# Performance work log

Measured on AMD Instinct MI355X. Metric: run time of the kernel, lower is better.

## Reference

```python
import jax, jax.numpy as jnp
import numpy as np

B, NV, HID, TDIM = 1024, 256, 256, 128
NODE_IN = 2 + 4 + TDIM  # coords + pos_enc(4) + time_emb


def _sinusoidal_pos_emb(t, dim):
    # standard SinusoidalPosEmb: cat(sin, cos) of t * exp(-i*log(1e4)/(half-1))
    half = dim // 2
    freqs = jnp.exp(-np.log(10000.0) * jnp.arange(half, dtype=t.dtype) / (half - 1))
    ang = t[:, None] * freqs[None, :]
    return jnp.concatenate([jnp.sin(ang), jnp.cos(ang)], axis=-1)  # [B, dim]


def setup_inputs() -> dict:
    key = jax.random.key(0)
    ks = jax.random.split(key, 10)
    s = lambda fan_in: 1.0 / np.sqrt(fan_in)
    return {
        "x": jax.random.normal(ks[0], (B, NV * 2), dtype=jnp.float32),
        "t": jax.random.uniform(ks[1], (B,), dtype=jnp.float32) * 1000.0,
        "time_w": jax.random.normal(ks[2], (TDIM, TDIM), dtype=jnp.float32) * s(TDIM),
        "time_b": jnp.zeros((TDIM,), dtype=jnp.float32),
        "W0": jax.random.normal(ks[3], (NODE_IN, HID), dtype=jnp.float32) * s(NODE_IN),
        "b0": jnp.zeros((HID,), dtype=jnp.float32),
        "W1": jax.random.normal(ks[4], (HID, HID), dtype=jnp.float32) * s(HID),
        "b1": jnp.zeros((HID,), dtype=jnp.float32),
        "W2": jax.random.normal(ks[5], (HID, HID), dtype=jnp.float32) * s(HID),
        "b2": jnp.zeros((HID,), dtype=jnp.float32),
    }


def reference(x, t, time_w, time_b, W0, b0, W1, b1, W2, b2):
    Bsz, D = x.shape
    n = D // 2
    coords = x.reshape(Bsz, n, 2)  # [B, n, 2]

    # cycle positional features (pos_enc_dim=4): sin/cos of vertex angle + 2nd harmonic
    pos = jnp.arange(n, dtype=x.dtype)
    theta = (2.0 * jnp.pi) * pos / n
    pe = jnp.stack([jnp.sin(theta), jnp.cos(theta), jnp.sin(2.0 * theta), jnp.cos(2.0 * theta)], axis=-1)
    pe = jnp.broadcast_to(pe[None], (Bsz, n, 4))

    # time MLP: SinusoidalPosEmb -> Linear -> SiLU, broadcast to every node of the graph
    temb = jax.nn.silu(_sinusoidal_pos_emb(t, time_w.shape[0]) @ time_w + time_b)  # [B, TDIM]
    temb = jnp.broadcast_to(temb[:, None, :], (Bsz, n, temb.shape[-1]))

    h = jnp.concatenate([coords, pe, temb], axis=-1)  # [B, n, NODE_IN]

    # GCN layers over cycle adjacency with self-loops, symmetric-normalized (deg=3 -> 1/3).
    # Cycle structure: neighbors are prev/next vertex within each polygon -> jnp.roll on axis 1.
    for W, b in ((W0, b0), (W1, b1), (W2, b2)):
        s = h @ W + b  # support = x W + b
        agg = (s + jnp.roll(s, 1, axis=1) + jnp.roll(s, -1, axis=1)) / 3.0
        h = jax.nn.silu(agg)

    # mean pooling per graph (scatter_mean over graph_index == mean over vertex axis here)
    return h.mean(axis=1)  # [B, HID]
```

## Files before the change

### kernel.cpp

```cpp
#include <hip/hip_runtime.h>
#include <cstdint>

typedef __attribute__((ext_vector_type(8)))  short bf16x8;
typedef __attribute__((ext_vector_type(16))) float f32x16;
typedef __attribute__((ext_vector_type(4)))  int   i32x4;

__device__ __forceinline__ unsigned short f2bf(float x) {
  unsigned u = __float_as_uint(x);
  u += 0x7fffu + ((u >> 16) & 1u);
  return (unsigned short)(u >> 16);
}
__device__ __forceinline__ unsigned pk2bf(float lo, float hi) {
#if defined(__has_builtin)
#if __has_builtin(__builtin_amdgcn_cvt_pk_bf16_f32)
  auto v = __builtin_amdgcn_cvt_pk_bf16_f32(lo, hi);
  unsigned u; __builtin_memcpy(&u, &v, 4); return u;
#else
  return ((unsigned)f2bf(hi) << 16) | (unsigned)f2bf(lo);
#endif
#else
  return ((unsigned)f2bf(hi) << 16) | (unsigned)f2bf(lo);
#endif
}
__device__ __forceinline__ float silu_f(float v) {
  return v * __builtin_amdgcn_rcpf(1.0f + __expf(-v));
}

__device__ __forceinline__ float xchg32(float A, float B, int q) {
#if defined(__has_builtin)
#if __has_builtin(__builtin_amdgcn_permlane32_swap)
  auto r = __builtin_amdgcn_permlane32_swap(__float_as_uint(A), __float_as_uint(B),
                                            false, false);
  return __uint_as_float(q ? r[0] : r[1]);
#else
  return __shfl_xor(q ? A : B, 32);
#endif
#else
  return __shfl_xor(q ? A : B, 32);
#endif
}

__global__ void pack_kernel(const float* __restrict__ W0, const float* __restrict__ W1,
                            const float* __restrict__ W2,
                            unsigned short* __restrict__ packW) {
  __shared__ float ldsF[16][257];
  const int s = blockIdx.x, tid = threadIdx.x;
  const float* W; int KT, kmax, base, kt;
  if (s < 9)       { W = W0; KT = 9;  kmax = 134; base = 0;      kt = s; }
  else if (s < 25) { W = W1; KT = 16; kmax = 256; base = 36864;  kt = s - 9; }
  else             { W = W2; KT = 16; kmax = 256; base = 102400; kt = s - 25; }
  const int k0 = kt * 16;
#pragma unroll
  for (int i = 0; i < 8; ++i) {
    const int idx = i * 512 + tid;
    const int kl = idx >> 8, col = idx & 255;
    const int kg = k0 + kl;
    ldsF[kl][col] = (kg < kmax) ? W[kg * 256 + col] * 0.33333334f : 0.0f;
  }
  __syncthreads();
  const int g = tid >> 7, t = (tid >> 6) & 1, lane = tid & 63;
  const int col = g * 64 + t * 32 + (lane & 31);
  const int kb = 8 * (lane >> 5);
  unsigned u0 = pk2bf(ldsF[kb + 0][col], ldsF[kb + 1][col]);
  unsigned u1 = pk2bf(ldsF[kb + 2][col], ldsF[kb + 3][col]);
  unsigned u2 = pk2bf(ldsF[kb + 4][col], ldsF[kb + 5][col]);
  unsigned u3 = pk2bf(ldsF[kb + 6][col], ldsF[kb + 7][col]);
  unsigned short* dst = packW + base + g * (KT * 1024) + t * (KT * 512) + kt * 512 + lane * 8;
  i32x4 v = { (int)u0, (int)u1, (int)u2, (int)u3 };
  *(i32x4*)dst = v;
}


template <int ELAYER, bool DF, bool DL>
__device__ __forceinline__ void epi_pair(
    const int p, const f32x16* accEpi, const int q,
    const float recvI0, const float recvI1, const float recvX,
    const float extP, const float extN,
    const int epiSub, unsigned short* __restrict__ hbuf,
    const int* rowAddr, float& psum) {
  const int t = p >> 3, rp = (p & 7) * 2;
  float y0, y1;
  {
    const int r = rp;
    float prev;
    if (r > 0) prev = accEpi[t][r - 1];
    else       prev = q ? (t ? recvI1 : recvI0) : (t ? recvX : extP);
    y0 = silu_f(prev + accEpi[t][r] + accEpi[t][r + 1]);
  }
  {
    const int r = rp + 1;
    float next;
    if (r < 15) next = accEpi[t][r + 1];
    else        next = q ? (t ? extN : recvX) : (t ? recvI1 : recvI0);
    y1 = silu_f(accEpi[t][r - 1] + accEpi[t][r] + next);
  }
  const bool c0 = !(DF && t == 0 && rp == 0 && q == 0);
  const bool c1 = !(DL && t == 1 && rp == 14 && q == 1);
  if constexpr (ELAYER == 2) {
    if (c0) psum += y0;
    if (c1) psum += y1;
  } else {
    const unsigned u = pk2bf(y0, y1);
    char* bp = (char*)hbuf + (2 * epiSub + t) * 16384;
    if (c0) *(unsigned short*)(bp + rowAddr[rp])     = (unsigned short)u;
    if (c1) *(unsigned short*)(bp + rowAddr[rp + 1]) = (unsigned short)(u >> 16);
  }
}

template <int KT, int ELAYER, bool DOEPI, bool DF, bool DL>
__device__ __forceinline__ void fblock(
    unsigned short* __restrict__ hbuf, const int readSub, const int epiSub,
    const bf16x8* Bf, const int q, const int c, const float bias3,
    f32x16* accOut, const f32x16* accEpi,
    const float extP, const float extN,
    const int* rowAddr, float& psum) {
  float recvI0 = 0.f, recvI1 = 0.f, recvX = 0.f;
  if constexpr (DOEPI) {
    recvI0 = xchg32(accEpi[0][0],  accEpi[0][15], q);
    recvI1 = xchg32(accEpi[1][0],  accEpi[1][15], q);
    recvX  = xchg32(accEpi[0][15], accEpi[1][0],  q);
  }
#pragma unroll
  for (int t2 = 0; t2 < 2; ++t2)
#pragma unroll
    for (int j = 0; j < 16; ++j) accOut[t2][j] = bias3;
  const unsigned short* rb = hbuf + readSub * 16384 + c * 256;
#pragma unroll
  for (int kt = 0; kt < KT; ++kt) {
    const unsigned short* base = rb + (((2 * kt + q) ^ c) * 8);
    const bf16x8 a0 = *(const bf16x8*)(base);
    const bf16x8 a1 = *(const bf16x8*)(base + 8192);
    accOut[0] = __builtin_amdgcn_mfma_f32_32x32x16_bf16(a0, Bf[kt], accOut[0], 0, 0, 0);
    accOut[1] = __builtin_amdgcn_mfma_f32_32x32x16_bf16(a1, Bf[kt], accOut[1], 0, 0, 0);
    if constexpr (DOEPI) {
#pragma unroll
      for (int p = (kt * 16) / KT; p < ((kt + 1) * 16) / KT; ++p)
        epi_pair<ELAYER, DF, DL>(p, accEpi, q, recvI0, recvI1, recvX, extP, extN,
                                 epiSub, hbuf, rowAddr, psum);
    }
  }
}

template <int ELAYER>
__device__ __forceinline__ void epi_only(
    const f32x16* accEpi, const int q, const float extP, const float extN,
    const int epiSub, unsigned short* __restrict__ hbuf,
    const int* rowAddr, float& psum) {
  const float recvI0 = xchg32(accEpi[0][0],  accEpi[0][15], q);
  const float recvI1 = xchg32(accEpi[1][0],  accEpi[1][15], q);
  const float recvX  = xchg32(accEpi[0][15], accEpi[1][0],  q);
#pragma unroll
  for (int p = 0; p < 16; ++p)
    epi_pair<ELAYER, false, false>(p, accEpi, q, recvI0, recvI1, recvX, extP, extN,
                                   epiSub, hbuf, rowAddr, psum);
}

template <int ELAYER>
__device__ __forceinline__ void defer_last(
    const f32x16* accEpi, const float accNew00, const int epiSub,
    const int q, unsigned short* __restrict__ hbuf,
    const int* rowAddr, float& psum) {
  const float recv = xchg32(0.f, accNew00, q);
  const float y = silu_f(accEpi[1][14] + accEpi[1][15] + recv);
  if (q) {
    if constexpr (ELAYER == 2) psum += y;
    else *(unsigned short*)((char*)hbuf + (2 * epiSub + 1) * 16384 + rowAddr[15]) = f2bf(y);
  }
}

template <int ELAYER>
__device__ __forceinline__ void fix_node0(
    const float s255src, const float sv0, const float sv1,
    const int q, unsigned short* __restrict__ hbuf,
    const int* rowAddr, float& psum) {
  const float recv = xchg32(s255src, 0.f, q);
  const float y = silu_f(recv + sv0 + sv1);
  if (!q) {
    if constexpr (ELAYER == 2) psum += y;
    else *(unsigned short*)((char*)hbuf + rowAddr[0]) = f2bf(y);
  }
}

__global__ __launch_bounds__(512, 1) void poly_kernel(
    const float* __restrict__ x, const float* __restrict__ t,
    const float* __restrict__ tw, const float* __restrict__ tb,
    const unsigned short* __restrict__ packW,
    const float* __restrict__ B0, const float* __restrict__ B1,
    const float* __restrict__ B2, float* __restrict__ out) {
  __shared__ __align__(16) unsigned short hbuf[65536];
  __shared__ __align__(16) unsigned short tmpl[160];

  const int tid = threadIdx.x;
  const int w = tid >> 6, lane = tid & 63, q = lane >> 5, c = lane & 31;
  const int b = blockIdx.x;

  {
    float* scr = (float*)hbuf;
    if (tid < 128) {
      const float tv = t[b];
      const int i = tid & 63;
      const float f = expf(-0.14619588396823767f * (float)i);
      const float ang = tv * f;
      scr[tid] = (tid < 64) ? sinf(ang) : cosf(ang);
    }
    __syncthreads();
    {
      const int j = tid & 127, p = tid >> 7;
      float a = 0.f;
#pragma unroll 8
      for (int kk = 0; kk < 32; ++kk) a += scr[p * 32 + kk] * tw[(p * 32 + kk) * 128 + j];
      scr[128 + tid] = a;
    }
    __syncthreads();
    if (tid < 128) {
      const float a = tb[tid] + scr[128 + tid] + scr[256 + tid] + scr[384 + tid] + scr[512 + tid];
      tmpl[6 + tid] = f2bf(silu_f(a));
      if (tid < 6)  tmpl[tid] = 0;
      if (tid < 26) tmpl[134 + tid] = 0;
    }
    __syncthreads();
  }

#pragma unroll
  for (int i = 0; i < 9; ++i) {
    const int task = tid + i * 512;
    const int node = task & 255, slot = task >> 8;
    i32x4 d = *(const i32x4*)(tmpl + slot * 8);
    if (slot == 0) {
      const float2 xy = ((const float2*)x)[b * 256 + node];
      const float th = 0.024543692605870074f * (float)node;
      d.x = (int)pk2bf(xy.x, xy.y);
      d.y = (int)pk2bf(sinf(th), cosf(th));
      d.z = (int)pk2bf(sinf(2.f * th), cosf(2.f * th));
    }
    const int m = (node & 3) + 8 * ((node >> 2) & 3) + 4 * ((node >> 4) & 1);
    const int R = (node & ~31) | m;
    *(i32x4*)(hbuf + R * 256 + ((slot ^ m) * 8)) = d;
  }

  int rowAddr[16];
  const int slotW = 4 * w + (c >> 3), offW = (c & 7) * 2;
#pragma unroll
  for (int r = 0; r < 16; ++r) {
    const int row = (r & 3) + 8 * (r >> 2) + 4 * q;
    rowAddr[r] = row * 512 + ((slotW ^ row) * 16) + offW;
  }

  const unsigned short* pL0 = packW + (w >> 1) * (9 * 1024) + (w & 1) * (9 * 512);
  const unsigned short* pL1 = packW + 36864 + (w >> 1) * (16 * 1024) + (w & 1) * (16 * 512);
  const unsigned short* pL2 = packW + 102400 + (w >> 1) * (16 * 1024) + (w & 1) * (16 * 512);
  bf16x8 Bf[16];
#pragma unroll
  for (int kt = 0; kt < 9; ++kt) Bf[kt] = *(const bf16x8*)(pL0 + kt * 512 + lane * 8);
  const float b30 = B0[w * 32 + c] * 0.33333334f;
  const float b31 = B1[w * 32 + c] * 0.33333334f;
  const float b32 = B2[w * 32 + c] * 0.33333334f;
  __syncthreads();

  f32x16 accA[2], accB[2];
  float psum = 0.f, sv0, sv1, extP, extN;

  fblock<9, 0, false, false, false>(hbuf, 0, 0, Bf, q, c, b30, accA, accA, 0.f, 0.f, rowAddr, psum);
  sv0 = accA[0][0]; sv1 = accA[0][1];
  __syncthreads();
  fblock<9, 0, true, true, true>(hbuf, 1, 0, Bf, q, c, b30, accB, accA, 0.f, 0.f, rowAddr, psum);
  defer_last<0>(accA, accB[0][0], 0, q, hbuf, rowAddr, psum);
  extP = xchg32(accA[1][15], 0.f, q);
  __syncthreads();
  fblock<9, 0, true, false, true>(hbuf, 2, 1, Bf, q, c, b30, accA, accB, extP, 0.f, rowAddr, psum);
  defer_last<0>(accB, accA[0][0], 1, q, hbuf, rowAddr, psum);
  extP = xchg32(accB[1][15], 0.f, q);
  __syncthreads();
  fblock<9, 0, true, false, true>(hbuf, 3, 2, Bf, q, c, b30, accB, accA, extP, 0.f, rowAddr, psum);
  defer_last<0>(accA, accB[0][0], 2, q, hbuf, rowAddr, psum);
  fix_node0<0>(accB[1][15], sv0, sv1, q, hbuf, rowAddr, psum);
  extP = xchg32(accA[1][15], 0.f, q);
  extN = xchg32(0.f, sv0, q);
#pragma unroll
  for (int kt = 0; kt < 16; ++kt) Bf[kt] = *(const bf16x8*)(pL1 + kt * 512 + lane * 8);
  __syncthreads();

  fblock<16, 0, true, false, false>(hbuf, 0, 3, Bf, q, c, b31, accA, accB, extP, extN, rowAddr, psum);
  sv0 = accA[0][0]; sv1 = accA[0][1];
  __syncthreads();
  fblock<16, 1, true, true, true>(hbuf, 1, 0, Bf, q, c, b31, accB, accA, 0.f, 0.f, rowAddr, psum);
  defer_last<1>(accA, accB[0][0], 0, q, hbuf, rowAddr, psum);
  extP = xchg32(accA[1][15], 0.f, q);
  __syncthreads();
  fblock<16, 1, true, false, true>(hbuf, 2, 1, Bf, q, c, b31, accA, accB, extP, 0.f, rowAddr, psum);
  defer_last<1>(accB, accA[0][0], 1, q, hbuf, rowAddr, psum);
  extP = xchg32(accB[1][15], 0.f, q);
  __syncthreads();
  fblock<16, 1, true, false, true>(hbuf, 3, 2, Bf, q, c, b31, accB, accA, extP, 0.f, rowAddr, psum);
  defer_last<1>(accA, accB[0][0], 2, q, hbuf, rowAddr, psum);
  fix_node0<1>(accB[1][15], sv0, sv1, q, hbuf, rowAddr, psum);
  extP = xchg32(accA[1][15], 0.f, q);
  extN = xchg32(0.f, sv0, q);
#pragma unroll
  for (int kt = 0; kt < 16; ++kt) Bf[kt] = *(const bf16x8*)(pL2 + kt * 512 + lane * 8);
  __syncthreads();

  fblock<16, 1, true, false, false>(hbuf, 0, 3, Bf, q, c, b32, accA, accB, extP, extN, rowAddr, psum);
  sv0 = accA[0][0]; sv1 = accA[0][1];
  __syncthreads();
  fblock<16, 2, true, true, true>(hbuf, 1, 0, Bf, q, c, b32, accB, accA, 0.f, 0.f, rowAddr, psum);
  defer_last<2>(accA, accB[0][0], 0, q, hbuf, rowAddr, psum);
  extP = xchg32(accA[1][15], 0.f, q);
  fblock<16, 2, true, false, true>(hbuf, 2, 1, Bf, q, c, b32, accA, accB, extP, 0.f, rowAddr, psum);
  defer_last<2>(accB, accA[0][0], 1, q, hbuf, rowAddr, psum);
  extP = xchg32(accB[1][15], 0.f, q);
  fblock<16, 2, true, false, true>(hbuf, 3, 2, Bf, q, c, b32, accB, accA, extP, 0.f, rowAddr, psum);
  defer_last<2>(accA, accB[0][0], 2, q, hbuf, rowAddr, psum);
  fix_node0<2>(accB[1][15], sv0, sv1, q, hbuf, rowAddr, psum);
  extP = xchg32(accA[1][15], 0.f, q);
  extN = xchg32(0.f, sv0, q);
  epi_only<2>(accB, q, extP, extN, 3, hbuf, rowAddr, psum);

  const float s2 = psum + xchg32(psum, psum, q);
  if (q == 0) out[b * 256 + w * 32 + c] = s2 * (1.0f / 256.0f);
}

extern "C" void kernel_launch(void* const* d_in, const int* in_sizes, int n_in,
                              void* d_out, int out_size, void* d_ws, size_t ws_size,
                              hipStream_t stream) {
  const float* x  = (const float*)d_in[0];
  const float* t  = (const float*)d_in[1];
  const float* tw = (const float*)d_in[2];
  const float* tb = (const float*)d_in[3];
  const float* W0 = (const float*)d_in[4];
  const float* b0 = (const float*)d_in[5];
  const float* W1 = (const float*)d_in[6];
  const float* b1 = (const float*)d_in[7];
  const float* W2 = (const float*)d_in[8];
  const float* b2 = (const float*)d_in[9];

  unsigned short* packW = (unsigned short*)d_ws;
  float* out = (float*)d_out;

  pack_kernel<<<41, 512, 0, stream>>>(W0, W1, W2, packW);
  poly_kernel<<<1024, 512, 0, stream>>>(x, t, tw, tb, packW, b0, b1, b2, out);
}
```

Measured before the change: 186.3 us.

## Precompute per-graph constant layer-0 contribution and shrink layer-0 GEMM to K=16

```diff
diff --git a/kernel.cpp b/kernel.cpp
--- a/kernel.cpp
+++ b/kernel.cpp
@@ -79,21 +79,14 @@
     const int epiSub, unsigned short* __restrict__ hbuf,
     const int* rowAddr, float& psum) {
   const int t = p >> 3, rp = (p & 7) * 2;
-  float y0, y1;
-  {
-    const int r = rp;
-    float prev;
-    if (r > 0) prev = accEpi[t][r - 1];
-    else       prev = q ? (t ? recvI1 : recvI0) : (t ? recvX : extP);
-    y0 = silu_f(prev + accEpi[t][r] + accEpi[t][r + 1]);
-  }
-  {
-    const int r = rp + 1;
-    float next;
-    if (r < 15) next = accEpi[t][r + 1];
-    else        next = q ? (t ? extN : recvX) : (t ? recvI1 : recvI0);
-    y1 = silu_f(accEpi[t][r - 1] + accEpi[t][r] + next);
-  }
+  const float mid = accEpi[t][rp] + accEpi[t][rp + 1];
+  float prev, next;
+  if (rp > 0) prev = accEpi[t][rp - 1];
+  else        prev = q ? (t ? recvI1 : recvI0) : (t ? recvX : extP);
+  if (rp < 14) next = accEpi[t][rp + 2];
+  else         next = q ? (t ? extN : recvX) : (t ? recvI1 : recvI0);
+  const float y0 = silu_f(prev + mid);
+  const float y1 = silu_f(mid + next);
   const bool c0 = !(DF && t == 0 && rp == 0 && q == 0);
   const bool c1 = !(DL && t == 1 && rp == 14 && q == 1);
   if constexpr (ELAYER == 2) {
@@ -125,13 +118,18 @@
 #pragma unroll
     for (int j = 0; j < 16; ++j) accOut[t2][j] = bias3;
   const unsigned short* rb = hbuf + readSub * 16384 + c * 256;
+  bf16x8 a0 = *(const bf16x8*)(rb + ((q ^ c) * 8));
+  bf16x8 a1 = *(const bf16x8*)(rb + ((q ^ c) * 8) + 8192);
 #pragma unroll
   for (int kt = 0; kt < KT; ++kt) {
-    const unsigned short* base = rb + (((2 * kt + q) ^ c) * 8);
-    const bf16x8 a0 = *(const bf16x8*)(base);
-    const bf16x8 a1 = *(const bf16x8*)(base + 8192);
-    accOut[0] = __builtin_amdgcn_mfma_f32_32x32x16_bf16(a0, Bf[kt], accOut[0], 0, 0, 0);
-    accOut[1] = __builtin_amdgcn_mfma_f32_32x32x16_bf16(a1, Bf[kt], accOut[1], 0, 0, 0);
+    const bf16x8 u0 = a0, u1 = a1;
+    if (kt + 1 < KT) {
+      const unsigned short* nb = rb + (((2 * (kt + 1) + q) ^ c) * 8);
+      a0 = *(const bf16x8*)(nb);
+      a1 = *(const bf16x8*)(nb + 8192);
+    }
+    accOut[0] = __builtin_amdgcn_mfma_f32_32x32x16_bf16(u0, Bf[kt], accOut[0], 0, 0, 0);
+    accOut[1] = __builtin_amdgcn_mfma_f32_32x32x16_bf16(u1, Bf[kt], accOut[1], 0, 0, 0);
     if constexpr (DOEPI) {
 #pragma unroll
       for (int p = (kt * 16) / KT; p < ((kt + 1) * 16) / KT; ++p)
@@ -221,12 +219,33 @@
     __syncthreads();
   }
 
-#pragma unroll
-  for (int i = 0; i < 9; ++i) {
-    const int task = tid + i * 512;
-    const int node = task & 255, slot = task >> 8;
-    i32x4 d = *(const i32x4*)(tmpl + slot * 8);
-    if (slot == 0) {
+  const unsigned short* pL0 = packW + (w >> 1) * (9 * 1024) + (w & 1) * (9 * 512);
+  const unsigned short* pL1 = packW + 36864 + (w >> 1) * (16 * 1024) + (w & 1) * (16 * 512);
+  const unsigned short* pL2 = packW + 102400 + (w >> 1) * (16 * 1024) + (w & 1) * (16 * 512);
+  bf16x8 Bf[16];
+#pragma unroll
+  for (int kt = 0; kt < 9; ++kt) Bf[kt] = *(const bf16x8*)(pL0 + kt * 512 + lane * 8);
+  const float b30 = B0[w * 32 + c] * 0.33333334f;
+  const float b31 = B1[w * 32 + c] * 0.33333334f;
+  const float b32 = B2[w * 32 + c] * 0.33333334f;
+
+  float initL0;
+  {
+    f32x16 Ct;
+#pragma unroll
+    for (int j = 0; j < 16; ++j) Ct[j] = 0.f;
+#pragma unroll
+    for (int kt = 0; kt < 9; ++kt) {
+      const bf16x8 at = *(const bf16x8*)(tmpl + kt * 16 + q * 8);
+      Ct = __builtin_amdgcn_mfma_f32_32x32x16_bf16(at, Bf[kt], Ct, 0, 0, 0);
+    }
+    initL0 = Ct[0] + b30;
+  }
+
+  {
+    const int node = tid >> 1, sl = tid & 1;
+    i32x4 d = {0, 0, 0, 0};
+    if (sl == 0) {
       const float2 xy = ((const float2*)x)[b * 256 + node];
       const float th = 0.024543692605870074f * (float)node;
       d.x = (int)pk2bf(xy.x, xy.y);
@@ -235,7 +254,7 @@
     }
     const int m = (node & 3) + 8 * ((node >> 2) & 3) + 4 * ((node >> 4) & 1);
     const int R = (node & ~31) | m;
-    *(i32x4*)(hbuf + R * 256 + ((slot ^ m) * 8)) = d;
+    *(i32x4*)(hbuf + R * 256 + ((sl ^ m) * 8)) = d;
   }
 
   int rowAddr[16];
@@ -245,33 +264,23 @@
     const int row = (r & 3) + 8 * (r >> 2) + 4 * q;
     rowAddr[r] = row * 512 + ((slotW ^ row) * 16) + offW;
   }
-
-  const unsigned short* pL0 = packW + (w >> 1) * (9 * 1024) + (w & 1) * (9 * 512);
-  const unsigned short* pL1 = packW + 36864 + (w >> 1) * (16 * 1024) + (w & 1) * (16 * 512);
-  const unsigned short* pL2 = packW + 102400 + (w >> 1) * (16 * 1024) + (w & 1) * (16 * 512);
-  bf16x8 Bf[16];
-#pragma unroll
-  for (int kt = 0; kt < 9; ++kt) Bf[kt] = *(const bf16x8*)(pL0 + kt * 512 + lane * 8);
-  const float b30 = B0[w * 32 + c] * 0.33333334f;
-  const float b31 = B1[w * 32 + c] * 0.33333334f;
-  const float b32 = B2[w * 32 + c] * 0.33333334f;
   __syncthreads();
 
   f32x16 accA[2], accB[2];
   float psum = 0.f, sv0, sv1, extP, extN;
 
-  fblock<9, 0, false, false, false>(hbuf, 0, 0, Bf, q, c, b30, accA, accA, 0.f, 0.f, rowAddr, psum);
+  fblock<1, 0, false, false, false>(hbuf, 0, 0, Bf, q, c, initL0, accA, accA, 0.f, 0.f, rowAddr, psum);
   sv0 = accA[0][0]; sv1 = accA[0][1];
   __syncthreads();
-  fblock<9, 0, true, true, true>(hbuf, 1, 0, Bf, q, c, b30, accB, accA, 0.f, 0.f, rowAddr, psum);
+  fblock<1, 0, true, true, true>(hbuf, 1, 0, Bf, q, c, initL0, accB, accA, 0.f, 0.f, rowAddr, psum);
   defer_last<0>(accA, accB[0][0], 0, q, hbuf, rowAddr, psum);
   extP = xchg32(accA[1][15], 0.f, q);
   __syncthreads();
-  fblock<9, 0, true, false, true>(hbuf, 2, 1, Bf, q, c, b30, accA, accB, extP, 0.f, rowAddr, psum);
+  fblock<1, 0, true, false, true>(hbuf, 2, 1, Bf, q, c, initL0, accA, accB, extP, 0.f, rowAddr, psum);
   defer_last<0>(accB, accA[0][0], 1, q, hbuf, rowAddr, psum);
   extP = xchg32(accB[1][15], 0.f, q);
   __syncthreads();
-  fblock<9, 0, true, false, true>(hbuf, 3, 2, Bf, q, c, b30, accB, accA, extP, 0.f, rowAddr, psum);
+  fblock<1, 0, true, false, true>(hbuf, 3, 2, Bf, q, c, initL0, accB, accA, extP, 0.f, rowAddr, psum);
   defer_last<0>(accA, accB[0][0], 2, q, hbuf, rowAddr, psum);
   fix_node0<0>(accB[1][15], sv0, sv1, q, hbuf, rowAddr, psum);
   extP = xchg32(accA[1][15], 0.f, q);
```

Result: faster. 176.3 us (-5.4%).
